# Kernel optimization log

Hardware: AMD Instinct MI355X
Metric: run time of the kernel (lower is better)

## Reference

```python
import jax, jax.numpy as jnp
import numpy as np

H, W = 256, 832            # full-res organized point cloud (HEIGHT/WIDTH globals)
STRIDE_H, STRIDE_W = 2, 4  # stride_H_list[0], stride_W_list[0]
OUT_H, OUT_W = 128, 208    # out_H_list[0], out_W_list[0]
KH, KW = 12, 20            # layer0 kernel_size
K = 32                     # layer0 K_sample


def _sa_layer(pts, h_idx, w_idx, w1, b1, w2, b2, w3, b3):
    """PointNet SA: strided center selection, window KNN grouping, MLP, max-pool.
    pts: (B,H,W,3); h_idx/w_idx: (M,) full-res grid coords of selected centers.
    """
    B = pts.shape[0]
    pts_flat = pts.reshape(B, H * W, 3)
    center_idx = h_idx * W + w_idx                      # (M,)
    centers = pts_flat[:, center_idx]                   # (B,M,3)  fast_select gather
    # candidate window around each center (clipped at borders)
    dh = jnp.arange(KH) - KH // 2
    dw = jnp.arange(KW) - KW // 2
    cand_h = jnp.clip(h_idx[:, None] + dh, 0, H - 1)    # (M,KH)
    cand_w = jnp.clip(w_idx[:, None] + dw, 0, W - 1)    # (M,KW)
    cand_idx = (cand_h[:, :, None] * W + cand_w[:, None, :]).reshape(-1, KH * KW)  # (M,P)
    cand = pts_flat[:, cand_idx]                        # (B,M,P,3) irregular gather
    d2 = jnp.sum((cand - centers[:, :, None, :]) ** 2, axis=-1)  # (B,M,P)
    _, nn = jax.lax.top_k(-d2, K)                       # K nearest within window
    knn = jnp.take_along_axis(cand, nn[..., None], axis=2)       # (B,M,K,3)
    rel = knn - centers[:, :, None, :]                  # local coordinates
    h = jax.nn.relu(rel @ w1 + b1)                      # mlp [8,8,16]
    h = jax.nn.relu(h @ w2 + b2)
    h = jax.nn.relu(h @ w3 + b3)
    return centers, jnp.max(h, axis=2)                  # (B,M,3), (B,M,16)


def setup_inputs() -> dict:
    key = jax.random.key(0)
    ks = jax.random.split(key, 5)
    return {
        "pos1": jax.random.normal(ks[0], (2, H, W, 3), jnp.float32) * 5.0,
        "pos2": jax.random.normal(ks[1], (2, H, W, 3), jnp.float32) * 5.0,
        "w1": jax.random.normal(ks[2], (3, 8), jnp.float32) * 0.3,
        "b1": jnp.zeros((8,), jnp.float32),
        "w2": jax.random.normal(ks[3], (8, 8), jnp.float32) * 0.3,
        "b2": jnp.zeros((8,), jnp.float32),
        "w3": jax.random.normal(ks[4], (8, 16), jnp.float32) * 0.3,
        "b3": jnp.zeros((16,), jnp.float32),
    }


def reference(pos1, pos2, w1, b1, w2, b2, w3, b3):
    # get_selected_idx for level 0: strided grid subsampling
    h_idx = jnp.repeat(jnp.arange(OUT_H) * STRIDE_H, OUT_W)  # (M,)
    w_idx = jnp.tile(jnp.arange(OUT_W) * STRIDE_W, OUT_H)    # (M,)
    _, f1 = _sa_layer(pos1, h_idx, w_idx, w1, b1, w2, b2, w3, b3)
    _, f2 = _sa_layer(pos2, h_idx, w_idx, w1, b1, w2, b2, w3, b3)
    return jnp.concatenate([f1, f2], axis=-1)  # (B, OUT_H*OUT_W, 32)
```

## Files before the change

kernel.cpp:

```cpp
#include <hip/hip_runtime.h>
#include <hip/hip_bf16.h>

#define HH 256
#define WW 832
#define OHH 128
#define OWW 208
#define NCAND 240
#define MM (OHH*OWW)

typedef float v2f __attribute__((ext_vector_type(2)));
typedef unsigned long long ull;

__device__ __forceinline__ int iclamp(int v, int lo, int hi) { return min(max(v, lo), hi); }
__device__ __forceinline__ int mbcnt2(ull m) {
    return __builtin_amdgcn_mbcnt_hi((unsigned)(m >> 32),
           __builtin_amdgcn_mbcnt_lo((unsigned)m, 0));
}
__device__ __forceinline__ v2f sxor(v2f v, int m) {
    v2f r; r.x = __shfl_xor(v.x, m); r.y = __shfl_xor(v.y, m); return r;
}
__device__ __forceinline__ v2f lo2(float4 f) { return (v2f){f.x, f.y}; }
__device__ __forceinline__ v2f hi2(float4 f) { return (v2f){f.z, f.w}; }

__global__ void __launch_bounds__(256) sa_fused(
    const float* __restrict__ pos1, const float* __restrict__ pos2,
    const float* __restrict__ w1, const float* __restrict__ b1,
    const float* __restrict__ w2, const float* __restrict__ b2,
    const float* __restrict__ w3, const float* __restrict__ b3,
    float* __restrict__ out)
{
    __shared__ float4 sW1q[3][2];
    __shared__ float4 sW2q[8][2];
    __shared__ float4 sW3q[8][4];
    __shared__ float4 sB1q[2], sB2q[2], sB3q[4];
    __shared__ int selJ[256];

    const int t = threadIdx.x;
    if (t < 6)            { int i = t >> 1, qd = (t & 1) * 4;
        sW1q[i][t & 1] = make_float4(w1[i*8+qd], w1[i*8+qd+1], w1[i*8+qd+2], w1[i*8+qd+3]); }
    if (t >= 8 && t < 24) { int u = t - 8, i = u >> 1, qd = (u & 1) * 4;
        sW2q[i][u & 1] = make_float4(w2[i*8+qd], w2[i*8+qd+1], w2[i*8+qd+2], w2[i*8+qd+3]); }
    if (t >= 32 && t < 64){ int u = t - 32, i = u >> 2, qd = (u & 3) * 4;
        sW3q[i][u & 3] = make_float4(w3[i*16+qd], w3[i*16+qd+1], w3[i*16+qd+2], w3[i*16+qd+3]); }
    if (t >= 64 && t < 66){ int u = (t - 64) * 4; sB1q[t-64] = make_float4(b1[u], b1[u+1], b1[u+2], b1[u+3]); }
    if (t >= 66 && t < 68){ int u = (t - 66) * 4; sB2q[t-66] = make_float4(b2[u], b2[u+1], b2[u+2], b2[u+3]); }
    if (t >= 68 && t < 72){ int u = (t - 68) * 4; sB3q[t-68] = make_float4(b3[u], b3[u+1], b3[u+2], b3[u+3]); }
    __syncthreads();

    const int lane = t & 63;
    const int wid  = t >> 6;
    const int l31  = lane & 31;
    const int half = lane >> 5;
    const int mA   = blockIdx.x * 8 + wid * 2;
    const int b    = blockIdx.y & 1;
    const int cl   = blockIdx.y >> 1;
    const float* __restrict__ base = (cl ? pos2 : pos1) + (size_t)b * (HH * WW * 3);

    int kh  = (lane * 3277) >> 14;
    int kwb = (lane - kh * 5) * 4;
    if (lane >= 60) { kh = 11; kwb = 0; }

    unsigned dA0, dA1, dA2, dA3, dB0, dB1, dB2, dB3;
    int h0A, w0A, h0B, w0B;
    float cxA, cyA, czA, cxB, cyB, czB;

    auto distpass = [&](int m, unsigned& D0, unsigned& D1, unsigned& D2, unsigned& D3,
                        int& h0o, int& w0o, float& cxo, float& cyo, float& czo) {
        const int oh = (int)(((unsigned)(m >> 4) * 5042u) >> 16);
        const int ow = m - oh * OWW;
        const int h0 = oh * 2, w0 = ow * 4;
        h0o = h0; w0o = w0;
        const float cx = base[(h0 * WW + w0) * 3 + 0];
        const float cy = base[(h0 * WW + w0) * 3 + 1];
        const float cz = base[(h0 * WW + w0) * 3 + 2];
        cxo = cx; cyo = cy; czo = cz;
        unsigned d2b[4];
        const bool interior = ((unsigned)(oh - 3) <= 122u) && ((unsigned)(ow - 3) <= 202u);
        if (interior) {
            const float* p = base + ((h0 - 6 + kh) * WW + (w0 - 10 + kwb)) * 3;
            float2 Av = *(const float2*)(p);
            float4 Bv = *(const float4*)(p + 2);
            float4 Cv = *(const float4*)(p + 6);
            float2 Dv = *(const float2*)(p + 10);
            float px[4] = {Av.x, Bv.y, Cv.x, Cv.w};
            float py[4] = {Av.y, Bv.z, Cv.y, Dv.x};
            float pz[4] = {Bv.x, Bv.w, Cv.z, Dv.y};
            #pragma unroll
            for (int q = 0; q < 4; ++q) {
                float dx = __fsub_rn(px[q], cx);
                float dy = __fsub_rn(py[q], cy);
                float dz = __fsub_rn(pz[q], cz);
                d2b[q] = __float_as_uint(__fadd_rn(__fadd_rn(__fmul_rn(dx, dx), __fmul_rn(dy, dy)), __fmul_rn(dz, dz)));
            }
        } else {
            int chh = iclamp(h0 - 6 + kh, 0, HH - 1);
            #pragma unroll
            for (int q = 0; q < 4; ++q) {
                int cw = iclamp(w0 - 10 + kwb + q, 0, WW - 1);
                const float* p = base + (chh * WW + cw) * 3;
                float dx = __fsub_rn(p[0], cx);
                float dy = __fsub_rn(p[1], cy);
                float dz = __fsub_rn(p[2], cz);
                d2b[q] = __float_as_uint(__fadd_rn(__fadd_rn(__fmul_rn(dx, dx), __fmul_rn(dy, dy)), __fmul_rn(dz, dz)));
            }
        }
        if (lane >= 60) { d2b[0] = d2b[1] = d2b[2] = d2b[3] = 0xFFFFFFFFu; }
        D0 = d2b[0]; D1 = d2b[1]; D2 = d2b[2]; D3 = d2b[3];
    };
    distpass(mA,     dA0, dA1, dA2, dA3, h0A, w0A, cxA, cyA, czA);
    distpass(mA + 1, dB0, dB1, dB2, dB3, h0B, w0B, cxB, cyB, czB);

    unsigned TA = 0, TB = 0; int c0A = 0, c0B = 0;
    bool exactA = false, exactB = false;
    ull svA0 = 0, svA1 = 0, svA2 = 0, svA3 = 0;
    ull svB0 = 0, svB1 = 0, svB2 = 0, svB3 = 0;
    for (int bpos = 30; bpos >= 0; --bpos) {
        if (!exactA) {
            unsigned Q = TA | (1u << bpos);
            ull t0 = __ballot(dA0 < Q);
            ull t1 = __ballot(dA1 < Q);
            ull t2 = __ballot(dA2 < Q);
            ull t3 = __ballot(dA3 < Q);
            int c = __popcll(t0) + __popcll(t1) + __popcll(t2) + __popcll(t3);
            if (c == 32) { TA = Q; exactA = true; svA0 = t0; svA1 = t1; svA2 = t2; svA3 = t3; }
            else if (c < 32) { TA = Q; c0A = c; }
        }
        if (!exactB) {
            unsigned Q = TB | (1u << bpos);
            ull t0 = __ballot(dB0 < Q);
            ull t1 = __ballot(dB1 < Q);
            ull t2 = __ballot(dB2 < Q);
            ull t3 = __ballot(dB3 < Q);
            int c = __popcll(t0) + __popcll(t1) + __popcll(t2) + __popcll(t3);
            if (c == 32) { TB = Q; exactB = true; svB0 = t0; svB1 = t1; svB2 = t2; svB3 = t3; }
            else if (c < 32) { TB = Q; c0B = c; }
        }
        if (exactA && exactB) break;
    }

    {
        bool m0, m1, m2, m3; ull s0, s1, s2, s3;
        if (exactA) {
            m0 = (dA0 < TA); m1 = (dA1 < TA); m2 = (dA2 < TA); m3 = (dA3 < TA);
            s0 = svA0; s1 = svA1; s2 = svA2; s3 = svA3;
        } else {
            const int r = 32 - c0A;
            bool eq0 = (dA0 == TA), eq1 = (dA1 == TA), eq2 = (dA2 == TA), eq3 = (dA3 == TA);
            ull e0 = __ballot(eq0), e1 = __ballot(eq1), e2 = __ballot(eq2), e3 = __ballot(eq3);
            int SA = mbcnt2(e0) + mbcnt2(e1) + mbcnt2(e2) + mbcnt2(e3);
            int E1 = (int)eq0, E2 = E1 + (int)eq1, E3 = E2 + (int)eq2;
            m0 = (dA0 < TA) || (eq0 && (SA      < r));
            m1 = (dA1 < TA) || (eq1 && (SA + E1 < r));
            m2 = (dA2 < TA) || (eq2 && (SA + E2 < r));
            m3 = (dA3 < TA) || (eq3 && (SA + E3 < r));
            s0 = __ballot(m0); s1 = __ballot(m1); s2 = __ballot(m2); s3 = __ballot(m3);
        }
        int p1 = __popcll(s0), p2 = p1 + __popcll(s1), p3 = p2 + __popcll(s2);
        int lb = wid * 64;
        int j4 = lane * 4;
        if (m0) selJ[lb +      mbcnt2(s0)] = j4;
        if (m1) selJ[lb + p1 + mbcnt2(s1)] = j4 + 1;
        if (m2) selJ[lb + p2 + mbcnt2(s2)] = j4 + 2;
        if (m3) selJ[lb + p3 + mbcnt2(s3)] = j4 + 3;
    }
    {
        bool m0, m1, m2, m3; ull s0, s1, s2, s3;
        if (exactB) {
            m0 = (dB0 < TB); m1 = (dB1 < TB); m2 = (dB2 < TB); m3 = (dB3 < TB);
            s0 = svB0; s1 = svB1; s2 = svB2; s3 = svB3;
        } else {
            const int r = 32 - c0B;
            bool eq0 = (dB0 == TB), eq1 = (dB1 == TB), eq2 = (dB2 == TB), eq3 = (dB3 == TB);
            ull e0 = __ballot(eq0), e1 = __ballot(eq1), e2 = __ballot(eq2), e3 = __ballot(eq3);
            int SA = mbcnt2(e0) + mbcnt2(e1) + mbcnt2(e2) + mbcnt2(e3);
            int E1 = (int)eq0, E2 = E1 + (int)eq1, E3 = E2 + (int)eq2;
            m0 = (dB0 < TB) || (eq0 && (SA      < r));
            m1 = (dB1 < TB) || (eq1 && (SA + E1 < r));
            m2 = (dB2 < TB) || (eq2 && (SA + E2 < r));
            m3 = (dB3 < TB) || (eq3 && (SA + E3 < r));
            s0 = __ballot(m0); s1 = __ballot(m1); s2 = __ballot(m2); s3 = __ballot(m3);
        }
        int p1 = __popcll(s0), p2 = p1 + __popcll(s1), p3 = p2 + __popcll(s2);
        int lb = wid * 64 + 32;
        int j4 = lane * 4;
        if (m0) selJ[lb +      mbcnt2(s0)] = j4;
        if (m1) selJ[lb + p1 + mbcnt2(s1)] = j4 + 1;
        if (m2) selJ[lb + p2 + mbcnt2(s2)] = j4 + 2;
        if (m3) selJ[lb + p3 + mbcnt2(s3)] = j4 + 3;
    }
    asm volatile("s_waitcnt lgkmcnt(0)" ::: "memory");
    __builtin_amdgcn_sched_barrier(0);

    {
        int jj = selJ[wid * 64 + lane];
        int L  = jj >> 2, q = jj & 3;
        int kh2 = (L * 3277) >> 14;
        int kw2 = (L - kh2 * 5) * 4 + q;
        int h0s = half ? h0B : h0A;
        int w0s = half ? w0B : w0A;
        int ch = iclamp(h0s - 6 + kh2, 0, HH - 1);
        int cw = iclamp(w0s - 10 + kw2, 0, WW - 1);
        const float* p = base + (ch * WW + cw) * 3;
        float rx = __fsub_rn(p[0], half ? cxB : cxA);
        float ry = __fsub_rn(p[1], half ? cyB : cyA);
        float rz = __fsub_rn(p[2], half ? czB : czA);
        v2f rx2 = (v2f){rx, rx};
        v2f ry2 = (v2f){ry, ry};
        v2f rz2 = (v2f){rz, rz};

        v2f a1[4];
        {
            float4 bq0 = sB1q[0], bq1 = sB1q[1];
            float4 x0 = sW1q[0][0], x1 = sW1q[0][1];
            float4 y0 = sW1q[1][0], y1 = sW1q[1][1];
            float4 z0 = sW1q[2][0], z1 = sW1q[2][1];
            a1[0] = __builtin_elementwise_fma(rx2, lo2(x0), lo2(bq0));
            a1[1] = __builtin_elementwise_fma(rx2, hi2(x0), hi2(bq0));
            a1[2] = __builtin_elementwise_fma(rx2, lo2(x1), lo2(bq1));
            a1[3] = __builtin_elementwise_fma(rx2, hi2(x1), hi2(bq1));
            a1[0] = __builtin_elementwise_fma(ry2, lo2(y0), a1[0]);
            a1[1] = __builtin_elementwise_fma(ry2, hi2(y0), a1[1]);
            a1[2] = __builtin_elementwise_fma(ry2, lo2(y1), a1[2]);
            a1[3] = __builtin_elementwise_fma(ry2, hi2(y1), a1[3]);
            a1[0] = __builtin_elementwise_fma(rz2, lo2(z0), a1[0]);
            a1[1] = __builtin_elementwise_fma(rz2, hi2(z0), a1[1]);
            a1[2] = __builtin_elementwise_fma(rz2, lo2(z1), a1[2]);
            a1[3] = __builtin_elementwise_fma(rz2, hi2(z1), a1[3]);
            #pragma unroll
            for (int op = 0; op < 4; ++op) a1[op] = __builtin_elementwise_max(a1[op], (v2f)(0.f));
        }
        v2f a2[4] = {lo2(sB2q[0]), hi2(sB2q[0]), lo2(sB2q[1]), hi2(sB2q[1])};
        #pragma unroll
        for (int i = 0; i < 8; ++i) {
            float h = a1[i >> 1][i & 1];
            v2f hb = (v2f){h, h};
            float4 wl = sW2q[i][0], wh = sW2q[i][1];
            a2[0] = __builtin_elementwise_fma(hb, lo2(wl), a2[0]);
            a2[1] = __builtin_elementwise_fma(hb, hi2(wl), a2[1]);
            a2[2] = __builtin_elementwise_fma(hb, lo2(wh), a2[2]);
            a2[3] = __builtin_elementwise_fma(hb, hi2(wh), a2[3]);
        }
        #pragma unroll
        for (int op = 0; op < 4; ++op) a2[op] = __builtin_elementwise_max(a2[op], (v2f)(0.f));

        v2f a3[8] = {lo2(sB3q[0]), hi2(sB3q[0]), lo2(sB3q[1]), hi2(sB3q[1]),
                     lo2(sB3q[2]), hi2(sB3q[2]), lo2(sB3q[3]), hi2(sB3q[3])};
        #pragma unroll
        for (int i = 0; i < 8; ++i) {
            float h = a2[i >> 1][i & 1];
            v2f hb = (v2f){h, h};
            float4 q0 = sW3q[i][0], q1 = sW3q[i][1], q2 = sW3q[i][2], q3 = sW3q[i][3];
            a3[0] = __builtin_elementwise_fma(hb, lo2(q0), a3[0]);
            a3[1] = __builtin_elementwise_fma(hb, hi2(q0), a3[1]);
            a3[2] = __builtin_elementwise_fma(hb, lo2(q1), a3[2]);
            a3[3] = __builtin_elementwise_fma(hb, hi2(q1), a3[3]);
            a3[4] = __builtin_elementwise_fma(hb, lo2(q2), a3[4]);
            a3[5] = __builtin_elementwise_fma(hb, hi2(q2), a3[5]);
            a3[6] = __builtin_elementwise_fma(hb, lo2(q3), a3[6]);
            a3[7] = __builtin_elementwise_fma(hb, hi2(q3), a3[7]);
        }

        #pragma unroll
        for (int step = 16; step >= 1; step >>= 1) {
            #pragma unroll
            for (int op = 0; op < 8; ++op)
                a3[op] = __builtin_elementwise_max(a3[op], sxor(a3[op], step));
        }
        if (l31 == 0) {
            #pragma unroll
            for (int op = 0; op < 8; ++op)
                a3[op] = __builtin_elementwise_max(a3[op], (v2f)(0.f));
            const int ms = mA + half;
            float4* dst = (float4*)(out + ((size_t)(b * MM + ms) * 32) + (size_t)cl * 16);
            dst[0] = make_float4(a3[0].x, a3[0].y, a3[1].x, a3[1].y);
            dst[1] = make_float4(a3[2].x, a3[2].y, a3[3].x, a3[3].y);
            dst[2] = make_float4(a3[4].x, a3[4].y, a3[5].x, a3[5].y);
            dst[3] = make_float4(a3[6].x, a3[6].y, a3[7].x, a3[7].y);
        }
    }
}

extern "C" void kernel_launch(void* const* d_in, const int* in_sizes, int n_in,
                              void* d_out, int out_size, void* d_ws, size_t ws_size,
                              hipStream_t stream) {
    const float* pos1 = (const float*)d_in[0];
    const float* pos2 = (const float*)d_in[1];
    const float* w1   = (const float*)d_in[2];
    const float* b1   = (const float*)d_in[3];
    const float* w2   = (const float*)d_in[4];
    const float* b2   = (const float*)d_in[5];
    const float* w3   = (const float*)d_in[6];
    const float* b3   = (const float*)d_in[7];
    float* out = (float*)d_out;

    dim3 grid(MM / 8, 4);
    sa_fused<<<grid, 256, 0, stream>>>(pos1, pos2, w1, b1, w2, b2, w3, b3, out);
}
```

Before: 88.91 us.

## Stage shared candidate window in LDS per wave for both centers

Each wave now loads one 12x24-point window covering the overlapping candidate regions of its two adjacent centers into shared memory, then computes distances and the final neighbor gather from LDS instead of issuing separate global loads per center. This removes redundant global reads, since the two 12x20 windows overlap heavily, and replaces the scattered global gather of selected neighbors with LDS reads. It adds LDS usage per block (about 14 KB), which may lower occupancy, and adds a staging phase before the distance pass.

New measurement: 99.01 us. 11.4% more time.

```diff
diff --git a/kernel.cpp b/kernel.cpp
--- a/kernel.cpp
+++ b/kernel.cpp
@@ -33,6 +33,7 @@
     __shared__ float4 sW2q[8][2];
     __shared__ float4 sW3q[8][4];
     __shared__ float4 sB1q[2], sB2q[2], sB3q[4];
+    __shared__ float4 sWin4[4][217];
     __shared__ int selJ[256];
 
     const int t = threadIdx.x;
@@ -56,59 +57,76 @@
     const int cl   = blockIdx.y >> 1;
     const float* __restrict__ base = (cl ? pos2 : pos1) + (size_t)b * (HH * WW * 3);
 
+    const int oh = (int)(((unsigned)(mA >> 4) * 5042u) >> 16);
+    const int ow = mA - oh * OWW;
+    const int h0 = oh * 2, w0 = ow * 4;
+
+    float* __restrict__ win = (float*)&sWin4[wid][0];
+
     int kh  = (lane * 3277) >> 14;
     int kwb = (lane - kh * 5) * 4;
     if (lane >= 60) { kh = 11; kwb = 0; }
 
+    const bool interior = ((unsigned)(oh - 3) <= 122u) && ((unsigned)(ow - 3) <= 201u);
+    if (interior) {
+        #pragma unroll
+        for (int rd = 0; rd < 4; ++rd) {
+            int chunk = rd * 64 + lane;
+            if (chunk < 216) {
+                int r  = (chunk * 3641) >> 16;
+                int k4 = (chunk - r * 18) * 4;
+                const float* g = base + ((h0 - 6 + r) * WW + (w0 - 10)) * 3 + k4;
+                float2 a = *(const float2*)g;
+                float2 c = *(const float2*)(g + 2);
+                sWin4[wid][chunk] = make_float4(a.x, a.y, c.x, c.y);
+            }
+        }
+    } else {
+        #pragma unroll
+        for (int rd = 0; rd < 5; ++rd) {
+            int pi = rd * 64 + lane;
+            if (pi < 288) {
+                int r = (pi * 2731) >> 16;
+                int c = pi - r * 24;
+                int gh = iclamp(h0 - 6 + r, 0, HH - 1);
+                int gw = iclamp(w0 - 10 + c, 0, WW - 1);
+                const float* g = base + (gh * WW + gw) * 3;
+                win[pi * 3 + 0] = g[0];
+                win[pi * 3 + 1] = g[1];
+                win[pi * 3 + 2] = g[2];
+            }
+        }
+    }
+    asm volatile("s_waitcnt lgkmcnt(0)" ::: "memory");
+    __builtin_amdgcn_sched_barrier(0);
+
     unsigned dA0, dA1, dA2, dA3, dB0, dB1, dB2, dB3;
-    int h0A, w0A, h0B, w0B;
     float cxA, cyA, czA, cxB, cyB, czB;
-
-    auto distpass = [&](int m, unsigned& D0, unsigned& D1, unsigned& D2, unsigned& D3,
-                        int& h0o, int& w0o, float& cxo, float& cyo, float& czo) {
-        const int oh = (int)(((unsigned)(m >> 4) * 5042u) >> 16);
-        const int ow = m - oh * OWW;
-        const int h0 = oh * 2, w0 = ow * 4;
-        h0o = h0; w0o = w0;
-        const float cx = base[(h0 * WW + w0) * 3 + 0];
-        const float cy = base[(h0 * WW + w0) * 3 + 1];
-        const float cz = base[(h0 * WW + w0) * 3 + 2];
-        cxo = cx; cyo = cy; czo = cz;
-        unsigned d2b[4];
-        const bool interior = ((unsigned)(oh - 3) <= 122u) && ((unsigned)(ow - 3) <= 202u);
-        if (interior) {
-            const float* p = base + ((h0 - 6 + kh) * WW + (w0 - 10 + kwb)) * 3;
-            float2 Av = *(const float2*)(p);
-            float4 Bv = *(const float4*)(p + 2);
-            float4 Cv = *(const float4*)(p + 6);
-            float2 Dv = *(const float2*)(p + 10);
-            float px[4] = {Av.x, Bv.y, Cv.x, Cv.w};
-            float py[4] = {Av.y, Bv.z, Cv.y, Dv.x};
-            float pz[4] = {Bv.x, Bv.w, Cv.z, Dv.y};
-            #pragma unroll
-            for (int q = 0; q < 4; ++q) {
-                float dx = __fsub_rn(px[q], cx);
-                float dy = __fsub_rn(py[q], cy);
-                float dz = __fsub_rn(pz[q], cz);
-                d2b[q] = __float_as_uint(__fadd_rn(__fadd_rn(__fmul_rn(dx, dx), __fmul_rn(dy, dy)), __fmul_rn(dz, dz)));
-            }
-        } else {
-            int chh = iclamp(h0 - 6 + kh, 0, HH - 1);
-            #pragma unroll
-            for (int q = 0; q < 4; ++q) {
-                int cw = iclamp(w0 - 10 + kwb + q, 0, WW - 1);
-                const float* p = base + (chh * WW + cw) * 3;
-                float dx = __fsub_rn(p[0], cx);
-                float dy = __fsub_rn(p[1], cy);
-                float dz = __fsub_rn(p[2], cz);
-                d2b[q] = __float_as_uint(__fadd_rn(__fadd_rn(__fmul_rn(dx, dx), __fmul_rn(dy, dy)), __fmul_rn(dz, dz)));
-            }
-        }
-        if (lane >= 60) { d2b[0] = d2b[1] = d2b[2] = d2b[3] = 0xFFFFFFFFu; }
-        D0 = d2b[0]; D1 = d2b[1]; D2 = d2b[2]; D3 = d2b[3];
-    };
-    distpass(mA,     dA0, dA1, dA2, dA3, h0A, w0A, cxA, cyA, czA);
-    distpass(mA + 1, dB0, dB1, dB2, dB3, h0B, w0B, cxB, cyB, czB);
+    #pragma unroll
+    for (int cc = 0; cc < 2; ++cc) {
+        const float* cptr = win + (154 + 4 * cc) * 3;
+        float cx = cptr[0], cy = cptr[1], cz = cptr[2];
+        const float* lp = win + (kh * 24 + kwb + 4 * cc) * 3;
+        float4 v0 = *(const float4*)(lp);
+        float4 v1 = *(const float4*)(lp + 4);
+        float4 v2 = *(const float4*)(lp + 8);
+        float px[4] = {v0.x, v0.w, v1.z, v2.y};
+        float py[4] = {v0.y, v1.x, v1.w, v2.z};
+        float pz[4] = {v0.z, v1.y, v2.x, v2.w};
+        unsigned dd[4];
+        #pragma unroll
+        for (int q = 0; q < 4; ++q) {
+            float dx = __fsub_rn(px[q], cx);
+            float dy = __fsub_rn(py[q], cy);
+            float dz = __fsub_rn(pz[q], cz);
+            dd[q] = __float_as_uint(__fadd_rn(__fadd_rn(__fmul_rn(dx, dx), __fmul_rn(dy, dy)), __fmul_rn(dz, dz)));
+        }
+        if (lane >= 60) { dd[0] = dd[1] = dd[2] = dd[3] = 0xFFFFFFFFu; }
+        if (cc == 0) { dA0 = dd[0]; dA1 = dd[1]; dA2 = dd[2]; dA3 = dd[3];
+                       cxA = cx; cyA = cy; czA = cz; }
+        else         { dB0 = dd[0]; dB1 = dd[1]; dB2 = dd[2]; dB3 = dd[3];
+                       cxB = cx; cyB = cy; czB = cz; }
+    }
 
     unsigned TA = 0, TB = 0; int c0A = 0, c0B = 0;
     bool exactA = false, exactB = false;
@@ -196,11 +214,7 @@
         int L  = jj >> 2, q = jj & 3;
         int kh2 = (L * 3277) >> 14;
         int kw2 = (L - kh2 * 5) * 4 + q;
-        int h0s = half ? h0B : h0A;
-        int w0s = half ? w0B : w0A;
-        int ch = iclamp(h0s - 6 + kh2, 0, HH - 1);
-        int cw = iclamp(w0s - 10 + kw2, 0, WW - 1);
-        const float* p = base + (ch * WW + cw) * 3;
+        const float* p = win + (kh2 * 24 + kw2 + 4 * half) * 3;
         float rx = __fsub_rn(p[0], half ? cxB : cxA);
         float ry = __fsub_rn(p[1], half ? cyB : cyA);
         float rz = __fsub_rn(p[2], half ? czB : czA);
```
